# Performance work log

Measured on AMD Instinct MI355X. Metric: run time of the kernel, lower is better.

Reference implementation:

```python
import jax, jax.numpy as jnp
import numpy as np

B, N, DIM = 64, 512, 128
LEAKY_ALPHA = 0.2
NEG_INF = -9e15


def setup_inputs() -> dict:
    key = jax.random.key(0)
    ks = jax.random.split(key, 9)
    stdv = 1.0 / np.sqrt(DIM)
    hidden = jax.random.normal(ks[0], (B, N, DIM), dtype=jnp.float32)
    adj = jax.random.randint(ks[1], (B, N, N), 0, 5, dtype=jnp.int32)
    input_times = jax.random.uniform(ks[2], (B, N), dtype=jnp.float32)
    # attention parameters a_0..a_3, each (dim,) (original stores (dim,1))
    a0 = jax.random.uniform(ks[3], (DIM,), minval=-stdv, maxval=stdv, dtype=jnp.float32)
    a1 = jax.random.uniform(ks[4], (DIM,), minval=-stdv, maxval=stdv, dtype=jnp.float32)
    a2 = jax.random.uniform(ks[5], (DIM,), minval=-stdv, maxval=stdv, dtype=jnp.float32)
    a3 = jax.random.uniform(ks[6], (DIM,), minval=-stdv, maxval=stdv, dtype=jnp.float32)
    # 'exp*' decay kernel params: p0 ~ U(0,0.01), p1 ~ U(0,1), then reset to U(-stdv,stdv)
    p0 = jax.random.uniform(ks[7], (1,), minval=-stdv, maxval=stdv, dtype=jnp.float32)
    p1 = jax.random.uniform(ks[8], (1,), minval=-stdv, maxval=stdv, dtype=jnp.float32)
    return {"hidden": hidden, "adj": adj, "input_times": input_times,
            "a0": a0, "a1": a1, "a2": a2, "a3": a3, "p0": p0, "p1": p1}


def reference(hidden, adj, input_times, a0, a1, a2, a3, p0, p1):
    # time embedding from 'exp*' kernel: p0 * exp(-t) + p1 -> [B, N, 1]
    te = p0 * jnp.exp(-input_times) + p1
    # drop last feature of hidden, append time embedding -> h: [B, N, dim]
    h = jnp.concatenate([hidden[:, :, :-1], te[:, :, None]], axis=2)

    def scores(a):
        # (h_i * h_j) . a == (h * a) @ h^T  -- avoids the O(B*N^2*dim) a_input
        e = jnp.einsum('bid,bjd->bij', h * a, h)
        return jax.nn.leaky_relu(e, LEAKY_ALPHA)

    e0, e1, e2, e3 = scores(a0), scores(a1), scores(a2), scores(a3)
    alpha = jnp.full_like(e0, NEG_INF)
    alpha = jnp.where(adj == 1, e0, alpha)
    alpha = jnp.where(adj == 2, e1, alpha)
    alpha = jnp.where(adj == 3, e2, alpha)
    alpha = jnp.where(adj == 4, e3, alpha)
    alpha = jax.nn.softmax(alpha, axis=-1)
    return jnp.einsum('bij,bjd->bid', alpha, h)
```

## Files before the change

kernel.cpp:

```cpp
#include <hip/hip_runtime.h>
#include <hip/hip_bf16.h>


typedef _Float16 half8  __attribute__((ext_vector_type(8)));
typedef _Float16 half4v __attribute__((ext_vector_type(4)));
typedef float    f32x4  __attribute__((ext_vector_type(4)));

namespace {
constexpr int kB = 64;
constexpr int kN = 512;
constexpr int kD = 128;
constexpr int TI = 128;
constexpr int TJ = 64;
constexpr float kNegInf = -9e15f;
constexpr float kAlpha  = 0.2f;
}

__launch_bounds__(512, 2)
__global__ void gat_mfma_f16(const float* __restrict__ hidden,
                             const int*   __restrict__ adj,
                             const float* __restrict__ times,
                             const float* __restrict__ a0,
                             const float* __restrict__ a1,
                             const float* __restrict__ a2,
                             const float* __restrict__ a3,
                             const float* __restrict__ p0p,
                             const float* __restrict__ p1p,
                             float* __restrict__ out)
{
    __shared__ _Float16 sh_hjh[TJ][136];
    __shared__ float    sh_hjf[TJ][132];
    __shared__ float    sh_p  [TI][68];
    __shared__ float    sh_scale[TI];
    __shared__ float    sh_l[TI];

    const int t    = threadIdx.x;
    const int b    = blockIdx.x >> 2;
    const int i0   = (blockIdx.x & 3) * TI;
    const int lane = t & 63;
    const int w    = t >> 6;
    const int g    = lane >> 4;
    const int c    = lane & 15;

    const float p0 = p0p[0];
    const float p1 = p1p[0];

    const int vx = t & 31;
    const int vy = t >> 5;

    half8 af[4][4];
    {
        const int arow = i0 + w * 16 + c;
        const float* hrow = hidden + ((size_t)b * kN + arow) * kD;
        const float te = p0 * __expf(-times[(size_t)b * kN + arow]) + p1;
#pragma unroll
        for (int kc = 0; kc < 4; ++kc) {
            const int d0 = kc * 32 + g * 8;
            f32x4 h0 = *reinterpret_cast<const f32x4*>(hrow + d0);
            f32x4 h1 = *reinterpret_cast<const f32x4*>(hrow + d0 + 4);
            if (d0 + 7 == 127) h1[3] = te;
            const float hv[8] = {h0[0], h0[1], h0[2], h0[3],
                                 h1[0], h1[1], h1[2], h1[3]};
            const float* aks[4] = {a0, a1, a2, a3};
#pragma unroll
            for (int k = 0; k < 4; ++k) {
                f32x4 A0 = *reinterpret_cast<const f32x4*>(aks[k] + d0);
                f32x4 A1 = *reinterpret_cast<const f32x4*>(aks[k] + d0 + 4);
                const float av[8] = {A0[0], A0[1], A0[2], A0[3],
                                     A1[0], A1[1], A1[2], A1[3]};
                half8 v;
#pragma unroll
                for (int r = 0; r < 8; ++r) v[r] = (_Float16)(hv[r] * av[r]);
                af[kc][k] = v;
            }
        }
    }

    float m_r[4], l_r[4];
#pragma unroll
    for (int q = 0; q < 4; ++q) { m_r[q] = kNegInf; l_r[q] = 0.f; }
    float o_acc[8][4];
#pragma unroll
    for (int r = 0; r < 8; ++r)
#pragma unroll
        for (int d = 0; d < 4; ++d) o_acc[r][d] = 0.f;

    for (int jt = 0; jt < 8; ++jt) {
        __syncthreads();

#pragma unroll
        for (int it = 0; it < 4; ++it) {
            const int flat = t + it * 512;
            const int row  = flat >> 5;
            const int c4   = flat & 31;
            const size_t jrow = (size_t)b * kN + jt * TJ + row;
            f32x4 v = *reinterpret_cast<const f32x4*>(hidden + jrow * kD + c4 * 4);
            if (c4 == 31) v[3] = p0 * __expf(-times[jrow]) + p1;
            *reinterpret_cast<f32x4*>(&sh_hjf[row][c4 * 4]) = v;
            half4v h;
#pragma unroll
            for (int x = 0; x < 4; ++x) h[x] = (_Float16)v[x];
            *reinterpret_cast<half4v*>(&sh_hjh[row][c4 * 4]) = h;
        }

        int adjv[4][4];
#pragma unroll
        for (int q = 0; q < 4; ++q)
#pragma unroll
            for (int jt4 = 0; jt4 < 4; ++jt4)
                adjv[q][jt4] = adj[((size_t)b * kN + i0 + w * 16 + g * 4 + q) * kN
                                   + jt * TJ + jt4 * 16 + c];

        __syncthreads();

        f32x4 E[4][4];
#pragma unroll
        for (int jt4 = 0; jt4 < 4; ++jt4)
#pragma unroll
            for (int k = 0; k < 4; ++k) E[jt4][k] = (f32x4)0.f;

#pragma unroll
        for (int kc = 0; kc < 4; ++kc) {
#pragma unroll
            for (int jt4 = 0; jt4 < 4; ++jt4) {
                half8 bf = *reinterpret_cast<const half8*>(
                    &sh_hjh[jt4 * 16 + c][kc * 32 + g * 8]);
#pragma unroll
                for (int k = 0; k < 4; ++k)
                    E[jt4][k] = __builtin_amdgcn_mfma_f32_16x16x32_f16(
                        af[kc][k], bf, E[jt4][k], 0, 0, 0);
            }
        }

#pragma unroll
        for (int q = 0; q < 4; ++q) {
            float vvq[4];
#pragma unroll
            for (int jt4 = 0; jt4 < 4; ++jt4) {
                const int k = adjv[q][jt4];
                const float e = (k == 1) ? E[jt4][0][q]
                              : (k == 2) ? E[jt4][1][q]
                              : (k == 3) ? E[jt4][2][q]
                              :            E[jt4][3][q];
                const float lr = fmaxf(e, 0.f) + kAlpha * fminf(e, 0.f);
                vvq[jt4] = (k == 0) ? kNegInf : lr;
            }
            float rm = fmaxf(fmaxf(vvq[0], vvq[1]), fmaxf(vvq[2], vvq[3]));
            rm = fmaxf(rm, __shfl_xor(rm, 1));
            rm = fmaxf(rm, __shfl_xor(rm, 2));
            rm = fmaxf(rm, __shfl_xor(rm, 4));
            rm = fmaxf(rm, __shfl_xor(rm, 8));
            const float mnew = fmaxf(m_r[q], rm);
            const float sc = __expf(m_r[q] - mnew);
            float pq[4];
#pragma unroll
            for (int jt4 = 0; jt4 < 4; ++jt4) pq[jt4] = __expf(vvq[jt4] - mnew);
            float ps = (pq[0] + pq[1]) + (pq[2] + pq[3]);
            ps += __shfl_xor(ps, 1);
            ps += __shfl_xor(ps, 2);
            ps += __shfl_xor(ps, 4);
            ps += __shfl_xor(ps, 8);
            l_r[q] = l_r[q] * sc + ps;
            m_r[q] = mnew;
            const int row = w * 16 + g * 4 + q;
#pragma unroll
            for (int jt4 = 0; jt4 < 4; ++jt4)
                sh_p[row][jt4 * 16 + c] = pq[jt4];
            if (c == 0) {
                sh_scale[row] = sc;
                if (jt == 7) sh_l[row] = l_r[q];
            }
        }
        __syncthreads();

#pragma unroll
        for (int r = 0; r < 8; ++r) {
            const float s = sh_scale[vy * 8 + r];
#pragma unroll
            for (int d = 0; d < 4; ++d) o_acc[r][d] *= s;
        }
#pragma unroll 2
        for (int j4 = 0; j4 < 16; ++j4) {
            f32x4 hv[4];
#pragma unroll
            for (int qq = 0; qq < 4; ++qq)
                hv[qq] = *reinterpret_cast<const f32x4*>(&sh_hjf[j4 * 4 + qq][vx * 4]);
#pragma unroll
            for (int r = 0; r < 8; ++r) {
                const f32x4 p4 = *reinterpret_cast<const f32x4*>(&sh_p[vy * 8 + r][j4 * 4]);
#pragma unroll
                for (int qq = 0; qq < 4; ++qq) {
#pragma unroll
                    for (int d = 0; d < 4; ++d)
                        o_acc[r][d] = fmaf(p4[qq], hv[qq][d], o_acc[r][d]);
                }
            }
        }
    }

#pragma unroll
    for (int r = 0; r < 8; ++r) {
        const int row = vy * 8 + r;
        const float inv = 1.0f / sh_l[row];
        f32x4 res;
#pragma unroll
        for (int d = 0; d < 4; ++d) res[d] = o_acc[r][d] * inv;
        *reinterpret_cast<f32x4*>(out + ((size_t)b * kN + i0 + row) * kD + vx * 4) = res;
    }
}

extern "C" void kernel_launch(void* const* d_in, const int* in_sizes, int n_in,
                              void* d_out, int out_size, void* d_ws, size_t ws_size,
                              hipStream_t stream) {
    const float* hidden = (const float*)d_in[0];
    const int*   adj    = (const int*)d_in[1];
    const float* times  = (const float*)d_in[2];
    const float* a0 = (const float*)d_in[3];
    const float* a1 = (const float*)d_in[4];
    const float* a2 = (const float*)d_in[5];
    const float* a3 = (const float*)d_in[6];
    const float* p0 = (const float*)d_in[7];
    const float* p1 = (const float*)d_in[8];
    float* outp = (float*)d_out;
    (void)in_sizes; (void)n_in; (void)out_size; (void)d_ws; (void)ws_size;

    gat_mfma_f16<<<dim3(kB * (kN / TI)), dim3(512), 0, stream>>>(
        hidden, adj, times, a0, a1, a2, a3, p0, p1, outp);
}
```

Measured before the change: 214.3 us.

## Move P·V aggregation onto MFMA with split-fp16 hi/lo values and smaller tiles

Replaces the scalar FP32 FMA loop for the softmax-weighted sum with f16 MFMA instructions. Hidden rows are stored transposed in LDS as hi and lo fp16 parts to keep near-fp32 accuracy, and probabilities are rounded to fp16. The block shrinks to 256 threads with 64 query rows, so there are twice as many blocks. This also removes one barrier per tile, since each wave keeps its own rows in registers. The costs are the transposed LDS stores, which may cause bank conflicts, and reduced precision in P.

```diff
diff --git a/kernel.cpp b/kernel.cpp
--- a/kernel.cpp
+++ b/kernel.cpp
@@ -10,33 +10,32 @@
 constexpr int kB = 64;
 constexpr int kN = 512;
 constexpr int kD = 128;
-constexpr int TI = 128;
+constexpr int TI = 64;
 constexpr int TJ = 64;
 constexpr float kNegInf = -9e15f;
 constexpr float kAlpha  = 0.2f;
 }
 
-__launch_bounds__(512, 2)
-__global__ void gat_mfma_f16(const float* __restrict__ hidden,
-                             const int*   __restrict__ adj,
-                             const float* __restrict__ times,
-                             const float* __restrict__ a0,
-                             const float* __restrict__ a1,
-                             const float* __restrict__ a2,
-                             const float* __restrict__ a3,
-                             const float* __restrict__ p0p,
-                             const float* __restrict__ p1p,
-                             float* __restrict__ out)
+__launch_bounds__(256, 2)
+__global__ void gat_mfma_full(const float* __restrict__ hidden,
+                              const int*   __restrict__ adj,
+                              const float* __restrict__ times,
+                              const float* __restrict__ a0,
+                              const float* __restrict__ a1,
+                              const float* __restrict__ a2,
+                              const float* __restrict__ a3,
+                              const float* __restrict__ p0p,
+                              const float* __restrict__ p1p,
+                              float* __restrict__ out)
 {
-    __shared__ _Float16 sh_hjh[TJ][136];
-    __shared__ float    sh_hjf[TJ][132];
-    __shared__ float    sh_p  [TI][68];
-    __shared__ float    sh_scale[TI];
-    __shared__ float    sh_l[TI];
+    __shared__ _Float16 sh_hjh  [TJ][136];
+    __shared__ _Float16 sh_hjT_hi[kD][72];
+    __shared__ _Float16 sh_hjT_lo[kD][72];
+    __shared__ _Float16 sh_p16 [TI][72];
 
     const int t    = threadIdx.x;
-    const int b    = blockIdx.x >> 2;
-    const int i0   = (blockIdx.x & 3) * TI;
+    const int b    = blockIdx.x >> 3;
+    const int i0   = (blockIdx.x & 7) * TI;
     const int lane = t & 63;
     const int w    = t >> 6;
     const int g    = lane >> 4;
@@ -44,9 +43,6 @@
 
     const float p0 = p0p[0];
     const float p1 = p1p[0];
-
-    const int vx = t & 31;
-    const int vy = t >> 5;
 
     half8 af[4][4];
     {
@@ -79,28 +75,35 @@
     float m_r[4], l_r[4];
 #pragma unroll
     for (int q = 0; q < 4; ++q) { m_r[q] = kNegInf; l_r[q] = 0.f; }
-    float o_acc[8][4];
-#pragma unroll
-    for (int r = 0; r < 8; ++r)
-#pragma unroll
-        for (int d = 0; d < 4; ++d) o_acc[r][d] = 0.f;
+    f32x4 o_acc[8];
+#pragma unroll
+    for (int nt = 0; nt < 8; ++nt) o_acc[nt] = (f32x4)0.f;
 
     for (int jt = 0; jt < 8; ++jt) {
         __syncthreads();
 
 #pragma unroll
-        for (int it = 0; it < 4; ++it) {
-            const int flat = t + it * 512;
+        for (int it = 0; it < 8; ++it) {
+            const int flat = t + it * 256;
             const int row  = flat >> 5;
             const int c4   = flat & 31;
             const size_t jrow = (size_t)b * kN + jt * TJ + row;
             f32x4 v = *reinterpret_cast<const f32x4*>(hidden + jrow * kD + c4 * 4);
             if (c4 == 31) v[3] = p0 * __expf(-times[jrow]) + p1;
-            *reinterpret_cast<f32x4*>(&sh_hjf[row][c4 * 4]) = v;
-            half4v h;
-#pragma unroll
-            for (int x = 0; x < 4; ++x) h[x] = (_Float16)v[x];
-            *reinterpret_cast<half4v*>(&sh_hjh[row][c4 * 4]) = h;
+            half4v hv, lv;
+#pragma unroll
+            for (int x = 0; x < 4; ++x) {
+                _Float16 h = (_Float16)v[x];
+                hv[x] = h;
+                lv[x] = (_Float16)(v[x] - (float)h);
+            }
+            *reinterpret_cast<half4v*>(&sh_hjh[row][c4 * 4]) = hv;
+            const int d0 = c4 * 4;
+#pragma unroll
+            for (int x = 0; x < 4; ++x) {
+                sh_hjT_hi[d0 + x][row] = hv[x];
+                sh_hjT_lo[d0 + x][row] = lv[x];
+            }
         }
 
         int adjv[4][4];
@@ -132,6 +135,7 @@
             }
         }
 
+        float scq[4];
 #pragma unroll
         for (int q = 0; q < 4; ++q) {
             float vvq[4];
@@ -152,60 +156,59 @@
             rm = fmaxf(rm, __shfl_xor(rm, 8));
             const float mnew = fmaxf(m_r[q], rm);
             const float sc = __expf(m_r[q] - mnew);
-            float pq[4];
-#pragma unroll
-            for (int jt4 = 0; jt4 < 4; ++jt4) pq[jt4] = __expf(vvq[jt4] - mnew);
-            float ps = (pq[0] + pq[1]) + (pq[2] + pq[3]);
+            half4v ph;
+            float pqf[4];
+#pragma unroll
+            for (int jt4 = 0; jt4 < 4; ++jt4) {
+                const float pv = __expf(vvq[jt4] - mnew);
+                const _Float16 h = (_Float16)pv;
+                ph[jt4]  = h;
+                pqf[jt4] = (float)h;
+            }
+            float ps = (pqf[0] + pqf[1]) + (pqf[2] + pqf[3]);
             ps += __shfl_xor(ps, 1);
             ps += __shfl_xor(ps, 2);
             ps += __shfl_xor(ps, 4);
             ps += __shfl_xor(ps, 8);
             l_r[q] = l_r[q] * sc + ps;
             m_r[q] = mnew;
-            const int row = w * 16 + g * 4 + q;
+            scq[q] = sc;
+            const int prow = w * 16 + g * 4 + q;
 #pragma unroll
             for (int jt4 = 0; jt4 < 4; ++jt4)
-                sh_p[row][jt4 * 16 + c] = pq[jt4];
-            if (c == 0) {
-                sh_scale[row] = sc;
-                if (jt == 7) sh_l[row] = l_r[q];
-            }
-        }
-        __syncthreads();
-
-#pragma unroll
-        for (int r = 0; r < 8; ++r) {
-            const float s = sh_scale[vy * 8 + r];
-#pragma unroll
-            for (int d = 0; d < 4; ++d) o_acc[r][d] *= s;
-        }
-#pragma unroll 2
-        for (int j4 = 0; j4 < 16; ++j4) {
-            f32x4 hv[4];
-#pragma unroll
-            for (int qq = 0; qq < 4; ++qq)
-                hv[qq] = *reinterpret_cast<const f32x4*>(&sh_hjf[j4 * 4 + qq][vx * 4]);
-#pragma unroll
-            for (int r = 0; r < 8; ++r) {
-                const f32x4 p4 = *reinterpret_cast<const f32x4*>(&sh_p[vy * 8 + r][j4 * 4]);
-#pragma unroll
-                for (int qq = 0; qq < 4; ++qq) {
-#pragma unroll
-                    for (int d = 0; d < 4; ++d)
-                        o_acc[r][d] = fmaf(p4[qq], hv[qq][d], o_acc[r][d]);
-                }
-            }
+                sh_p16[prow][jt4 * 16 + c] = ph[jt4];
+        }
+
+        half8 pA0 = *reinterpret_cast<const half8*>(&sh_p16[w * 16 + c][g * 8]);
+        half8 pA1 = *reinterpret_cast<const half8*>(&sh_p16[w * 16 + c][32 + g * 8]);
+#pragma unroll
+        for (int nt = 0; nt < 8; ++nt) {
+            f32x4 acc = o_acc[nt];
+            acc[0] *= scq[0]; acc[1] *= scq[1];
+            acc[2] *= scq[2]; acc[3] *= scq[3];
+            const int dd = nt * 16 + c;
+            half8 bh0 = *reinterpret_cast<const half8*>(&sh_hjT_hi[dd][g * 8]);
+            half8 bl0 = *reinterpret_cast<const half8*>(&sh_hjT_lo[dd][g * 8]);
+            half8 bh1 = *reinterpret_cast<const half8*>(&sh_hjT_hi[dd][32 + g * 8]);
+            half8 bl1 = *reinterpret_cast<const half8*>(&sh_hjT_lo[dd][32 + g * 8]);
+            acc = __builtin_amdgcn_mfma_f32_16x16x32_f16(pA0, bh0, acc, 0, 0, 0);
+            acc = __builtin_amdgcn_mfma_f32_16x16x32_f16(pA0, bl0, acc, 0, 0, 0);
+            acc = __builtin_amdgcn_mfma_f32_16x16x32_f16(pA1, bh1, acc, 0, 0, 0);
+            acc = __builtin_amdgcn_mfma_f32_16x16x32_f16(pA1, bl1, acc, 0, 0, 0);
+            o_acc[nt] = acc;
         }
     }
 
-#pragma unroll
-    for (int r = 0; r < 8; ++r) {
-        const int row = vy * 8 + r;
-        const float inv = 1.0f / sh_l[row];
-        f32x4 res;
-#pragma unroll
-        for (int d = 0; d < 4; ++d) res[d] = o_acc[r][d] * inv;
-        *reinterpret_cast<f32x4*>(out + ((size_t)b * kN + i0 + row) * kD + vx * 4) = res;
+    float inv[4];
+#pragma unroll
+    for (int q = 0; q < 4; ++q) inv[q] = 1.0f / l_r[q];
+#pragma unroll
+    for (int nt = 0; nt < 8; ++nt) {
+#pragma unroll
+        for (int q = 0; q < 4; ++q) {
+            const int row = i0 + w * 16 + g * 4 + q;
+            out[((size_t)b * kN + row) * kD + nt * 16 + c] = o_acc[nt][q] * inv[q];
+        }
     }
 }
 
@@ -224,6 +227,6 @@
     float* outp = (float*)d_out;
     (void)in_sizes; (void)n_in; (void)out_size; (void)d_ws; (void)ws_size;
 
-    gat_mfma_f16<<<dim3(kB * (kN / TI)), dim3(512), 0, stream>>>(
+    gat_mfma_full<<<dim3(kB * (kN / TI)), dim3(256), 0, stream>>>(
         hidden, adj, times, a0, a1, a2, a3, p0, p1, outp);
 }
```

Result: slower. 222.5 us (+3.8%).
